# Kernel tuning notes

Hardware: AMD Instinct MI355X
Metric: run time of the kernel (lower is better)

The kernel has to match this reference:

```python
import jax, jax.numpy as jnp
import numpy as np

B, N_FIELDS, D_IN, HID, HEADS = 1024, 32, 64, 128, 4
E_PER_G = 256
N_TOTAL = B * N_FIELDS


def setup_inputs() -> dict:
    key = jax.random.key(0)
    ks = jax.random.split(key, 12)
    # per-graph template edges, replicated with per-graph node offsets
    src_t = jax.random.randint(ks[0], (E_PER_G,), 0, N_FIELDS)
    dst_t = jax.random.randint(ks[1], (E_PER_G,), 0, N_FIELDS)
    offs = (jnp.arange(B) * N_FIELDS)[:, None]
    src = (src_t[None, :] + offs).reshape(-1)
    dst = (dst_t[None, :] + offs).reshape(-1)
    loops = jnp.arange(N_TOTAL)  # PyG GATConv add_self_loops=True
    edge_index = jnp.stack([jnp.concatenate([src, loops]),
                            jnp.concatenate([dst, loops])]).astype(jnp.int32)
    batch_idx = jnp.repeat(jnp.arange(B), N_FIELDS).astype(jnp.int32)

    def glorot(k, shape):
        fan = shape[0]
        return jax.random.normal(k, shape, jnp.float32) / np.float32(np.sqrt(fan))

    return {
        "x_fields": jax.random.normal(ks[2], (B, N_FIELDS, D_IN), jnp.float32),
        "aligner_w": glorot(ks[3], (D_IN, HID)),
        "aligner_b": jnp.zeros((HID,), jnp.float32),
        "ln_gamma": jnp.ones((HID,), jnp.float32),
        "ln_beta": jnp.zeros((HID,), jnp.float32),
        "gate_logits": jnp.full((N_FIELDS,), 2.2, jnp.float32),
        "w1": glorot(ks[4], (HID, HEADS * HID)),
        "att_src1": jax.random.normal(ks[5], (HEADS, HID), jnp.float32) * 0.1,
        "att_dst1": jax.random.normal(ks[6], (HEADS, HID), jnp.float32) * 0.1,
        "bias1": jnp.zeros((HEADS * HID,), jnp.float32),
        "w2": glorot(ks[7], (HEADS * HID, HID)),
        "att_src2": jax.random.normal(ks[8], (1, HID), jnp.float32) * 0.1,
        "att_dst2": jax.random.normal(ks[9], (1, HID), jnp.float32) * 0.1,
        "bias2": jnp.zeros((HID,), jnp.float32),
        "edge_index": edge_index,
        "batch_idx": batch_idx,
    }


def _gat(x, W, a_src, a_dst, bias, src, dst, heads, out_dim, concat):
    n = x.shape[0]
    h = (x @ W).reshape(n, heads, out_dim)          # [N,H,F]
    e_s = jnp.einsum('nhf,hf->nh', h, a_src)         # per-node src logits
    e_d = jnp.einsum('nhf,hf->nh', h, a_dst)
    logits = jax.nn.leaky_relu(e_s[src] + e_d[dst], 0.2)   # [E,H]
    # segment softmax over destination nodes (self-loops -> no empty segs)
    m = jax.ops.segment_max(logits, dst, num_segments=n)
    ex = jnp.exp(logits - m[dst])
    denom = jax.ops.segment_sum(ex, dst, num_segments=n)
    alpha = ex / denom[dst]
    out = jax.ops.segment_sum(h[src] * alpha[..., None], dst, num_segments=n)
    out = out.reshape(n, heads * out_dim) if concat else out.mean(axis=1)
    return out + bias


def reference(x_fields, aligner_w, aligner_b, ln_gamma, ln_beta, gate_logits,
              w1, att_src1, att_dst1, bias1, w2, att_src2, att_dst2, bias2,
              edge_index, batch_idx):
    # fused alignment: one Linear over all fields
    aligned = x_fields @ aligner_w + aligner_b       # [B,N,HID]
    mu = aligned.mean(-1, keepdims=True)
    var = ((aligned - mu) ** 2).mean(-1, keepdims=True)
    normed = (aligned - mu) / jnp.sqrt(var + 1e-5) * ln_gamma + ln_beta
    gate = jax.nn.sigmoid(gate_logits)               # [N]
    x = (normed * gate[None, :, None]).reshape(-1, HID)  # [B*N, HID]
    src, dst = edge_index[0], edge_index[1]
    x = _gat(x, w1, att_src1, att_dst1, bias1, src, dst, HEADS, HID, True)
    x = jax.nn.elu(x)
    x = _gat(x, w2, att_src2, att_dst2, bias2, src, dst, 1, HID, False)
    counts = jax.ops.segment_sum(jnp.ones((x.shape[0],), x.dtype), batch_idx,
                                 num_segments=B)
    graph_embedding = jax.ops.segment_sum(x, batch_idx, num_segments=B) / counts[:, None]
    return graph_embedding, gate
```

## Files before the change

kernel.cpp:

```cpp
#include <hip/hip_runtime.h>
#include <hip/hip_bf16.h>
#include <cstdint>
#include <cstddef>

#define NB    1024
#define NF    32
#define DIN   64
#define HID   128
#define HEADS 4
#define NTOT  (NB*NF)
#define H1DIM (HEADS*HID)

typedef __attribute__((ext_vector_type(8))) short          bf16x8;
typedef __attribute__((ext_vector_type(8))) unsigned short u16x8;
typedef __attribute__((ext_vector_type(4))) float          f32x4;

__device__ __forceinline__ float bf2f(unsigned short u) {
    return __uint_as_float(((unsigned)u) << 16);
}
__device__ __forceinline__ unsigned short f2bf(float f) {
    unsigned u = __float_as_uint(f);
    return (unsigned short)((u + 0x7FFF + ((u >> 16) & 1)) >> 16);
}

__device__ __forceinline__ int x0_at(int r, int c) {
    return r * 128 + ((((c >> 3) ^ (r & 7)) & 15) << 3) + (c & 7);
}
__device__ __forceinline__ int h1_at(int f, int s) {
    return f * 32 + ((((s >> 3) ^ ((f >> 1) & 3)) & 3) << 3) + (s & 7);
}
__device__ __forceinline__ int x1_at(int r, int c) {
    return r * 512 + ((((c >> 3) ^ ((r >> 1) & 7)) & 63) << 3) + (c & 7);
}
__device__ __forceinline__ int al_at(int rr, int s) {
    return rr * 32 + ((((s >> 3) ^ ((rr >> 1) & 3)) & 3) << 3) + (s & 7);
}

__global__ __launch_bounds__(256) void k_prep(
    const float* __restrict__ w1, const float* __restrict__ w2,
    const float* __restrict__ Wa,
    unsigned short* __restrict__ w1T, unsigned short* __restrict__ w2T,
    unsigned short* __restrict__ WaT)
{
    int i = blockIdx.x * 256 + threadIdx.x;
    if (i < HID * H1DIM) {
        int n = i >> 7, k = i & 127;
        w1T[i] = f2bf(w1[k * H1DIM + n]);
    } else if (i < 2 * HID * H1DIM) {
        int j = i - HID * H1DIM;
        int n = j >> 9, k = j & 511;
        w2T[j] = f2bf(w2[k * HID + n]);
    } else {
        int j = i - 2 * HID * H1DIM;
        int c = j >> 6, k = j & 63;
        WaT[j] = f2bf(Wa[k * HID + c]);
    }
}

__global__ __launch_bounds__(256, 3) void k_mega(
    const float* __restrict__ xf, const unsigned short* __restrict__ WaT,
    const float* __restrict__ ba, const float* __restrict__ gamma,
    const float* __restrict__ beta, const float* __restrict__ gl,
    const unsigned short* __restrict__ w1T, const float* __restrict__ as1,
    const float* __restrict__ ad1, const float* __restrict__ b1,
    const unsigned short* __restrict__ w2T, const float* __restrict__ as2,
    const float* __restrict__ ad2, const float* __restrict__ b2,
    const int* __restrict__ src, const int* __restrict__ dst, int epg,
    float* __restrict__ dout)
{
    __shared__ __align__(16) char S[54144];
    int*            cntI   = (int*)S;
    unsigned short* h1T    = (unsigned short*)S;
    unsigned short* x1L    = (unsigned short*)S;
    unsigned short* alphaL = (unsigned short*)(S + 32768);
    unsigned short* x0L    = (unsigned short*)(S + 40960);
    float*          aL2    = (float*)(S + 40960);
    unsigned char*  cntB   = (unsigned char*)(S + 49152);
    float* lnS   = (float*)(S + 50176);
    float* lnS2  = (float*)(S + 50688);
    float* esL   = (float*)(S + 51200);
    float* edL   = (float*)(S + 51712);
    float* rsumL = (float*)(S + 52224);
    float* es2p  = (float*)(S + 52736);
    float* ed2p  = (float*)(S + 53248);
    float* sc2   = (float*)(S + 53760);

    const int b = blockIdx.x, t = threadIdx.x;
    const int l = t & 63, w = t >> 6;
    const int g = l >> 4, i16 = l & 15;
    const int nb = b * NF;
    const f32x4 zf4 = {0.f, 0.f, 0.f, 0.f};

    for (int i = t; i < NF * NF; i += 256) cntI[i] = 0;
    __syncthreads();
    for (int i = t; i < epg; i += 256) {
        int sv = src[b * epg + i] - nb;
        int dv = dst[b * epg + i] - nb;
        atomicAdd(&cntI[dv * NF + sv], 1);
    }
    if (t < NF) atomicAdd(&cntI[t * NF + t], 1);
    __syncthreads();
    for (int i = t; i < NF * NF; i += 256) {
        int c = cntI[i];
        cntB[i] = (unsigned char)(c > 255 ? 255 : c);
    }
    __syncthreads();

    f32x4 accA[2][2];
    #pragma unroll
    for (int m = 0; m < 2; ++m)
        #pragma unroll
        for (int n = 0; n < 2; ++n) accA[m][n] = zf4;

    #pragma unroll
    for (int k = 0; k < 2; ++k) {
        bf16x8 aF[2];
        #pragma unroll
        for (int m = 0; m < 2; ++m) {
            const float* p = &xf[(size_t)(nb + m * 16 + i16) * DIN + k * 32 + g * 8];
            float4 f0 = *(const float4*)p;
            float4 f1 = *(const float4*)(p + 4);
            u16x8 v;
            v[0] = f2bf(f0.x); v[1] = f2bf(f0.y); v[2] = f2bf(f0.z); v[3] = f2bf(f0.w);
            v[4] = f2bf(f1.x); v[5] = f2bf(f1.y); v[6] = f2bf(f1.z); v[7] = f2bf(f1.w);
            aF[m] = (bf16x8)v;
        }
        #pragma unroll
        for (int n = 0; n < 2; ++n) {
            bf16x8 bF = *(const bf16x8*)&WaT[(size_t)(w * 32 + n * 16 + i16) * DIN + k * 32 + g * 8];
            #pragma unroll
            for (int m = 0; m < 2; ++m)
                accA[m][n] = __builtin_amdgcn_mfma_f32_16x16x32_bf16(aF[m], bF, accA[m][n], 0, 0, 0);
        }
    }
    float val[2][2][4];
    float bav[2];
    #pragma unroll
    for (int n = 0; n < 2; ++n) bav[n] = ba[w * 32 + n * 16 + i16];
    float ps[2][4], ps2[2][4];
    #pragma unroll
    for (int m = 0; m < 2; ++m)
        #pragma unroll
        for (int v = 0; v < 4; ++v) {
            float a0 = accA[m][0][v] + bav[0];
            float a1 = accA[m][1][v] + bav[1];
            val[m][0][v] = a0; val[m][1][v] = a1;
            ps[m][v] = a0 + a1;
            ps2[m][v] = a0 * a0 + a1 * a1;
        }
    #pragma unroll
    for (int o = 1; o < 16; o <<= 1) {
        #pragma unroll
        for (int m = 0; m < 2; ++m)
            #pragma unroll
            for (int v = 0; v < 4; ++v) {
                ps[m][v]  += __shfl_xor(ps[m][v], o);
                ps2[m][v] += __shfl_xor(ps2[m][v], o);
            }
    }
    if (i16 == 0) {
        #pragma unroll
        for (int m = 0; m < 2; ++m)
            #pragma unroll
            for (int v = 0; v < 4; ++v) {
                int r = m * 16 + g * 4 + v;
                lnS[w * 32 + r]  = ps[m][v];
                lnS2[w * 32 + r] = ps2[m][v];
            }
    }
    __syncthreads();
    #pragma unroll
    for (int m = 0; m < 2; ++m)
        #pragma unroll
        for (int v = 0; v < 4; ++v) {
            int r = m * 16 + g * 4 + v;
            float S1 = lnS[r] + lnS[32 + r] + lnS[64 + r] + lnS[96 + r];
            float S2 = lnS2[r] + lnS2[32 + r] + lnS2[64 + r] + lnS2[96 + r];
            float mu = S1 * (1.0f / HID);
            float var = S2 * (1.0f / HID) - mu * mu;
            float rs = rsqrtf(var + 1e-5f);
            float gt = 1.0f / (1.0f + __expf(-gl[r]));
            #pragma unroll
            for (int n = 0; n < 2; ++n) {
                int c = w * 32 + n * 16 + i16;
                float xv = ((val[m][n][v] - mu) * rs * gamma[c] + beta[c]) * gt;
                x0L[x0_at(r, c)] = f2bf(xv);
            }
        }
    __syncthreads();

    f32x4 acc1[2][8];
    #pragma unroll
    for (int m = 0; m < 2; ++m)
        #pragma unroll
        for (int n = 0; n < 8; ++n) acc1[m][n] = zf4;

    #pragma unroll 2
    for (int k = 0; k < 4; ++k) {
        bf16x8 aF[2];
        #pragma unroll
        for (int m = 0; m < 2; ++m)
            aF[m] = *(const bf16x8*)&x0L[x0_at(m * 16 + i16, k * 32 + g * 8)];
        #pragma unroll
        for (int n = 0; n < 8; ++n) {
            bf16x8 bF = *(const bf16x8*)&w1T[(size_t)(w * 128 + n * 16 + i16) * 128 + k * 32 + g * 8];
            #pragma unroll
            for (int m = 0; m < 2; ++m)
                acc1[m][n] = __builtin_amdgcn_mfma_f32_16x16x32_bf16(aF[m], bF, acc1[m][n], 0, 0, 0);
        }
    }
    {
        float asv[8], adv[8];
        #pragma unroll
        for (int n = 0; n < 8; ++n) {
            int f = n * 16 + i16;
            asv[n] = as1[w * 128 + f];
            adv[n] = ad1[w * 128 + f];
        }
        float pe[2][4], pd[2][4];
        #pragma unroll
        for (int m = 0; m < 2; ++m)
            #pragma unroll
            for (int v = 0; v < 4; ++v) {
                float e = 0.f, d = 0.f;
                #pragma unroll
                for (int n = 0; n < 8; ++n) {
                    e = fmaf(acc1[m][n][v], asv[n], e);
                    d = fmaf(acc1[m][n][v], adv[n], d);
                }
                pe[m][v] = e; pd[m][v] = d;
            }
        #pragma unroll
        for (int o = 1; o < 16; o <<= 1) {
            #pragma unroll
            for (int m = 0; m < 2; ++m)
                #pragma unroll
                for (int v = 0; v < 4; ++v) {
                    pe[m][v] += __shfl_xor(pe[m][v], o);
                    pd[m][v] += __shfl_xor(pd[m][v], o);
                }
        }
        if (i16 == 0) {
            #pragma unroll
            for (int m = 0; m < 2; ++m)
                #pragma unroll
                for (int v = 0; v < 4; ++v) {
                    int r = m * 16 + g * 4 + v;
                    esL[w * 32 + r] = pe[m][v];
                    edL[w * 32 + r] = pd[m][v];
                }
        }
        #pragma unroll
        for (int m = 0; m < 2; ++m)
            #pragma unroll
            for (int n = 0; n < 8; ++n) {
                int f = w * 128 + n * 16 + i16;
                int s0 = m * 16 + g * 4;
                unsigned d0 = (unsigned)f2bf(acc1[m][n][0]) | ((unsigned)f2bf(acc1[m][n][1]) << 16);
                unsigned d1 = (unsigned)f2bf(acc1[m][n][2]) | ((unsigned)f2bf(acc1[m][n][3]) << 16);
                uint2 pk = {d0, d1};
                *(uint2*)&h1T[h1_at(f, s0)] = pk;
            }
    }
    __syncthreads();

    if (t < 128) {
        int d = t >> 2, h = t & 3;
        float edv = edL[h * 32 + d];
        float mx = -INFINITY;
        #pragma unroll
        for (int s = 0; s < NF; ++s) {
            if (cntB[d * NF + s]) {
                float lg = esL[h * 32 + s] + edv;
                lg = fmaxf(lg, 0.2f * lg);
                mx = fmaxf(mx, lg);
            }
        }
        float sum = 0.f;
        #pragma unroll
        for (int s = 0; s < NF; ++s) {
            int c = cntB[d * NF + s];
            float a = 0.f;
            if (c) {
                float lg = esL[h * 32 + s] + edv;
                lg = fmaxf(lg, 0.2f * lg);
                a = (float)c * __expf(lg - mx);
                sum += a;
            }
            alphaL[al_at(h * 32 + d, s)] = f2bf(a);
        }
        rsumL[h * 32 + d] = 1.0f / sum;
    }
    __syncthreads();

    f32x4 po[2][8];
    {
        bf16x8 aF2[2];
        #pragma unroll
        for (int m = 0; m < 2; ++m)
            aF2[m] = *(const bf16x8*)&alphaL[al_at(w * 32 + m * 16 + i16, g * 8)];
        #pragma unroll
        for (int n = 0; n < 8; ++n) {
            bf16x8 bF = *(const bf16x8*)&h1T[h1_at(w * 128 + n * 16 + i16, g * 8)];
            #pragma unroll
            for (int m = 0; m < 2; ++m)
                po[m][n] = __builtin_amdgcn_mfma_f32_16x16x32_bf16(aF2[m], bF, zf4, 0, 0, 0);
        }
    }
    __syncthreads();
    #pragma unroll
    for (int m = 0; m < 2; ++m)
        #pragma unroll
        for (int n = 0; n < 8; ++n) {
            int c = w * 128 + n * 16 + i16;
            float bias = b1[c];
            #pragma unroll
            for (int v = 0; v < 4; ++v) {
                int r = m * 16 + g * 4 + v;
                float x = po[m][n][v] * rsumL[w * 32 + r] + bias;
                x = (x > 0.f) ? x : (__expf(x) - 1.0f);
                x1L[x1_at(r, c)] = f2bf(x);
            }
        }
    __syncthreads();

    f32x4 acc2[2][2];
    #pragma unroll
    for (int m = 0; m < 2; ++m)
        #pragma unroll
        for (int n = 0; n < 2; ++n) acc2[m][n] = zf4;

    #pragma unroll 4
    for (int k = 0; k < 16; ++k) {
        bf16x8 aF[2];
        #pragma unroll
        for (int m = 0; m < 2; ++m)
            aF[m] = *(const bf16x8*)&x1L[x1_at(m * 16 + i16, k * 32 + g * 8)];
        #pragma unroll
        for (int n = 0; n < 2; ++n) {
            bf16x8 bF = *(const bf16x8*)&w2T[(size_t)(w * 32 + n * 16 + i16) * 512 + k * 32 + g * 8];
            #pragma unroll
            for (int m = 0; m < 2; ++m)
                acc2[m][n] = __builtin_amdgcn_mfma_f32_16x16x32_bf16(aF[m], bF, acc2[m][n], 0, 0, 0);
        }
    }
    {
        float a2v[2], d2v[2];
        #pragma unroll
        for (int n = 0; n < 2; ++n) {
            int c = w * 32 + n * 16 + i16;
            a2v[n] = as2[c]; d2v[n] = ad2[c];
        }
        float pe[2][4], pd[2][4];
        #pragma unroll
        for (int m = 0; m < 2; ++m)
            #pragma unroll
            for (int v = 0; v < 4; ++v) {
                float e = 0.f, d = 0.f;
                #pragma unroll
                for (int n = 0; n < 2; ++n) {
                    e = fmaf(acc2[m][n][v], a2v[n], e);
                    d = fmaf(acc2[m][n][v], d2v[n], d);
                }
                pe[m][v] = e; pd[m][v] = d;
            }
        #pragma unroll
        for (int o = 1; o < 16; o <<= 1) {
            #pragma unroll
            for (int m = 0; m < 2; ++m)
                #pragma unroll
                for (int v = 0; v < 4; ++v) {
                    pe[m][v] += __shfl_xor(pe[m][v], o);
                    pd[m][v] += __shfl_xor(pd[m][v], o);
                }
        }
        if (i16 == 0) {
            #pragma unroll
            for (int m = 0; m < 2; ++m)
                #pragma unroll
                for (int v = 0; v < 4; ++v) {
                    int r = m * 16 + g * 4 + v;
                    es2p[w * 32 + r] = pe[m][v];
                    ed2p[w * 32 + r] = pd[m][v];
                }
        }
    }
    __syncthreads();

    float* es2L = sc2;
    float* ed2L = sc2 + 32;
    float* wn2  = sc2 + 64;
    if (t < NF) {
        es2L[t] = es2p[t] + es2p[32 + t] + es2p[64 + t] + es2p[96 + t];
        ed2L[t] = ed2p[t] + ed2p[32 + t] + ed2p[64 + t] + ed2p[96 + t];
    }
    __syncthreads();
    if (t < NF) {
        int d = t;
        float edv = ed2L[d];
        float mx = -INFINITY;
        #pragma unroll
        for (int s = 0; s < NF; ++s) {
            if (cntB[d * NF + s]) {
                float lg = es2L[s] + edv;
                lg = fmaxf(lg, 0.2f * lg);
                mx = fmaxf(mx, lg);
            }
        }
        float sum = 0.f;
        #pragma unroll
        for (int s = 0; s < NF; ++s) {
            int c = cntB[d * NF + s];
            float a = 0.f;
            if (c) {
                float lg = es2L[s] + edv;
                lg = fmaxf(lg, 0.2f * lg);
                a = (float)c * __expf(lg - mx);
                sum += a;
            }
            aL2[d * 33 + s] = a;
        }
        float rs = 1.0f / sum;
        #pragma unroll
        for (int s = 0; s < NF; ++s) aL2[d * 33 + s] *= rs;
    }
    __syncthreads();
    if (t < NF) {
        float a = 0.f;
        #pragma unroll
        for (int d = 0; d < NF; ++d) a += aL2[d * 33 + t];
        wn2[t] = a;
    }
    __syncthreads();

    {
        float wr_[2][4];
        #pragma unroll
        for (int m = 0; m < 2; ++m)
            #pragma unroll
            for (int v = 0; v < 4; ++v) wr_[m][v] = wn2[m * 16 + g * 4 + v];
        float pl[2];
        #pragma unroll
        for (int n = 0; n < 2; ++n) {
            float a = 0.f;
            #pragma unroll
            for (int m = 0; m < 2; ++m)
                #pragma unroll
                for (int v = 0; v < 4; ++v)
                    a = fmaf(wr_[m][v], acc2[m][n][v], a);
            pl[n] = a;
        }
        #pragma unroll
        for (int n = 0; n < 2; ++n) {
            pl[n] += __shfl_xor(pl[n], 16);
            pl[n] += __shfl_xor(pl[n], 32);
        }
        if (l < 16) {
            #pragma unroll
            for (int n = 0; n < 2; ++n) {
                int c = w * 32 + n * 16 + l;
                dout[(size_t)b * HID + c] = pl[n] * (1.0f / NF) + b2[c];
            }
        }
    }
    if (b == 0 && t < NF)
        dout[(size_t)NB * HID + t] = 1.0f / (1.0f + __expf(-gl[t]));
}

extern "C" void kernel_launch(void* const* d_in, const int* in_sizes, int n_in,
                              void* d_out, int out_size, void* d_ws, size_t ws_size,
                              hipStream_t stream)
{
    const float* xf    = (const float*)d_in[0];
    const float* Wa    = (const float*)d_in[1];
    const float* ba    = (const float*)d_in[2];
    const float* gamma = (const float*)d_in[3];
    const float* beta  = (const float*)d_in[4];
    const float* gl    = (const float*)d_in[5];
    const float* w1    = (const float*)d_in[6];
    const float* as1   = (const float*)d_in[7];
    const float* ad1   = (const float*)d_in[8];
    const float* b1    = (const float*)d_in[9];
    const float* w2    = (const float*)d_in[10];
    const float* as2   = (const float*)d_in[11];
    const float* ad2   = (const float*)d_in[12];
    const float* b2    = (const float*)d_in[13];
    const int*   eidx  = (const int*)d_in[14];
    const int E = in_sizes[14] / 2;
    const int* srcG = eidx;
    const int* dstG = eidx + E;
    const int epg = (E - NTOT) / NB;

    char* w = (char*)d_ws;
    unsigned short* w1T = (unsigned short*)w; w += (size_t)H1DIM * HID * 2;
    unsigned short* w2T = (unsigned short*)w; w += (size_t)HID * H1DIM * 2;
    unsigned short* WaT = (unsigned short*)w; w += (size_t)HID * DIN * 2;

    k_prep<<<(2 * HID * H1DIM + DIN * HID) / 256, 256, 0, stream>>>(
        w1, w2, Wa, w1T, w2T, WaT);

    k_mega<<<NB, 256, 0, stream>>>(
        xf, WaT, ba, gamma, beta, gl, w1T, as1, ad1, b1,
        w2T, as2, ad2, b2, srcG, dstG, epg, (float*)d_out);
}
```

Before: 158.8 us.

## Split fused GAT kernel into per-head layer-1 kernel and separate layer-2 kernel

Replaces the single per-graph mega kernel with two kernels. The first runs one 128-thread block per graph and head, recomputing the aligner and LayerNorm for each head, and writes the ELU output of GAT layer 1 to a global bf16 buffer. The second reads that buffer back for layer 2 and pooling. Both kernels spread the softmax across 128 threads using shuffle reductions, where previously only 32 or 128 threads did the serial loops. The aim is more blocks, smaller LDS use and higher occupancy, at the cost of redundant aligner and edge-count work per head and a global round trip of the 512-wide intermediate.

Result: slower. 164.7 us (+3.7%).

```diff
diff --git a/kernel.cpp b/kernel.cpp
--- a/kernel.cpp
+++ b/kernel.cpp
@@ -26,14 +26,14 @@
 __device__ __forceinline__ int x0_at(int r, int c) {
     return r * 128 + ((((c >> 3) ^ (r & 7)) & 15) << 3) + (c & 7);
 }
-__device__ __forceinline__ int h1_at(int f, int s) {
+__device__ __forceinline__ int hT_at(int f, int s) {
     return f * 32 + ((((s >> 3) ^ ((f >> 1) & 3)) & 3) << 3) + (s & 7);
+}
+__device__ __forceinline__ int al_at(int d, int s) {
+    return d * 32 + ((((s >> 3) ^ ((d >> 1) & 3)) & 3) << 3) + (s & 7);
 }
 __device__ __forceinline__ int x1_at(int r, int c) {
     return r * 512 + ((((c >> 3) ^ ((r >> 1) & 7)) & 63) << 3) + (c & 7);
-}
-__device__ __forceinline__ int al_at(int rr, int s) {
-    return rr * 32 + ((((s >> 3) ^ ((rr >> 1) & 3)) & 3) << 3) + (s & 7);
 }
 
 __global__ __launch_bounds__(256) void k_prep(
@@ -57,60 +57,55 @@
     }
 }
 
-__global__ __launch_bounds__(256, 3) void k_mega(
+__global__ __launch_bounds__(128) void k_gnn1(
     const float* __restrict__ xf, const unsigned short* __restrict__ WaT,
     const float* __restrict__ ba, const float* __restrict__ gamma,
     const float* __restrict__ beta, const float* __restrict__ gl,
     const unsigned short* __restrict__ w1T, const float* __restrict__ as1,
     const float* __restrict__ ad1, const float* __restrict__ b1,
-    const unsigned short* __restrict__ w2T, const float* __restrict__ as2,
-    const float* __restrict__ ad2, const float* __restrict__ b2,
     const int* __restrict__ src, const int* __restrict__ dst, int epg,
-    float* __restrict__ dout)
+    unsigned short* __restrict__ x1g)
 {
-    __shared__ __align__(16) char S[54144];
-    int*            cntI   = (int*)S;
+    __shared__ __align__(16) char S[14592];
+    unsigned short* x0L    = (unsigned short*)S;
     unsigned short* h1T    = (unsigned short*)S;
-    unsigned short* x1L    = (unsigned short*)S;
-    unsigned short* alphaL = (unsigned short*)(S + 32768);
-    unsigned short* x0L    = (unsigned short*)(S + 40960);
-    float*          aL2    = (float*)(S + 40960);
-    unsigned char*  cntB   = (unsigned char*)(S + 49152);
-    float* lnS   = (float*)(S + 50176);
-    float* lnS2  = (float*)(S + 50688);
-    float* esL   = (float*)(S + 51200);
-    float* edL   = (float*)(S + 51712);
-    float* rsumL = (float*)(S + 52224);
-    float* es2p  = (float*)(S + 52736);
-    float* ed2p  = (float*)(S + 53248);
-    float* sc2   = (float*)(S + 53760);
-
-    const int b = blockIdx.x, t = threadIdx.x;
-    const int l = t & 63, w = t >> 6;
+    unsigned short* x1Ls   = (unsigned short*)S;
+    int*            cntI   = (int*)(S + 8192);
+    unsigned short* alphaL = (unsigned short*)(S + 10240);
+    unsigned char*  cntB   = (unsigned char*)(S + 12288);
+    float* lnSp  = (float*)(S + 13312);
+    float* lnS2p = (float*)(S + 13568);
+    float* esP   = (float*)(S + 13824);
+    float* edP   = (float*)(S + 14080);
+    float* rsumL = (float*)(S + 14336);
+
+    const int bid = blockIdx.x;
+    const int b = bid >> 2, h = bid & 3;
+    const int t = threadIdx.x;
+    const int w2 = t >> 6, l = t & 63;
     const int g = l >> 4, i16 = l & 15;
     const int nb = b * NF;
     const f32x4 zf4 = {0.f, 0.f, 0.f, 0.f};
 
-    for (int i = t; i < NF * NF; i += 256) cntI[i] = 0;
-    __syncthreads();
-    for (int i = t; i < epg; i += 256) {
+    for (int i = t; i < NF * NF; i += 128) cntI[i] = 0;
+    __syncthreads();
+    for (int i = t; i < epg; i += 128) {
         int sv = src[b * epg + i] - nb;
         int dv = dst[b * epg + i] - nb;
         atomicAdd(&cntI[dv * NF + sv], 1);
     }
-    if (t < NF) atomicAdd(&cntI[t * NF + t], 1);
-    __syncthreads();
-    for (int i = t; i < NF * NF; i += 256) {
+    if (t < NF) atomicAdd(&cntI[t * 33], 1);
+    __syncthreads();
+    for (int i = t; i < NF * NF; i += 128) {
         int c = cntI[i];
         cntB[i] = (unsigned char)(c > 255 ? 255 : c);
     }
-    __syncthreads();
-
-    f32x4 accA[2][2];
+
+    f32x4 accA[2][4];
     #pragma unroll
     for (int m = 0; m < 2; ++m)
         #pragma unroll
-        for (int n = 0; n < 2; ++n) accA[m][n] = zf4;
+        for (int n = 0; n < 4; ++n) accA[m][n] = zf4;
 
     #pragma unroll
     for (int k = 0; k < 2; ++k) {
@@ -126,28 +121,31 @@
             aF[m] = (bf16x8)v;
         }
         #pragma unroll
-        for (int n = 0; n < 2; ++n) {
-            bf16x8 bF = *(const bf16x8*)&WaT[(size_t)(w * 32 + n * 16 + i16) * DIN + k * 32 + g * 8];
+        for (int n = 0; n < 4; ++n) {
+            bf16x8 bF = *(const bf16x8*)&WaT[(size_t)(w2 * 64 + n * 16 + i16) * DIN + k * 32 + g * 8];
             #pragma unroll
             for (int m = 0; m < 2; ++m)
                 accA[m][n] = __builtin_amdgcn_mfma_f32_16x16x32_bf16(aF[m], bF, accA[m][n], 0, 0, 0);
         }
     }
-    float val[2][2][4];
-    float bav[2];
-    #pragma unroll
-    for (int n = 0; n < 2; ++n) bav[n] = ba[w * 32 + n * 16 + i16];
+    float val[2][4][4];
     float ps[2][4], ps2[2][4];
     #pragma unroll
     for (int m = 0; m < 2; ++m)
         #pragma unroll
-        for (int v = 0; v < 4; ++v) {
-            float a0 = accA[m][0][v] + bav[0];
-            float a1 = accA[m][1][v] + bav[1];
-            val[m][0][v] = a0; val[m][1][v] = a1;
-            ps[m][v] = a0 + a1;
-            ps2[m][v] = a0 * a0 + a1 * a1;
-        }
+        for (int v = 0; v < 4; ++v) { ps[m][v] = 0.f; ps2[m][v] = 0.f; }
+    #pragma unroll
+    for (int n = 0; n < 4; ++n) {
+        float bav = ba[w2 * 64 + n * 16 + i16];
+        #pragma unroll
+        for (int m = 0; m < 2; ++m)
+            #pragma unroll
+            for (int v = 0; v < 4; ++v) {
+                float a = accA[m][n][v] + bav;
+                val[m][n][v] = a;
+                ps[m][v] += a; ps2[m][v] += a * a;
+            }
+    }
     #pragma unroll
     for (int o = 1; o < 16; o <<= 1) {
         #pragma unroll
@@ -164,8 +162,8 @@
             #pragma unroll
             for (int v = 0; v < 4; ++v) {
                 int r = m * 16 + g * 4 + v;
-                lnS[w * 32 + r]  = ps[m][v];
-                lnS2[w * 32 + r] = ps2[m][v];
+                lnSp[w2 * 32 + r]  = ps[m][v];
+                lnS2p[w2 * 32 + r] = ps2[m][v];
             }
     }
     __syncthreads();
@@ -174,48 +172,49 @@
         #pragma unroll
         for (int v = 0; v < 4; ++v) {
             int r = m * 16 + g * 4 + v;
-            float S1 = lnS[r] + lnS[32 + r] + lnS[64 + r] + lnS[96 + r];
-            float S2 = lnS2[r] + lnS2[32 + r] + lnS2[64 + r] + lnS2[96 + r];
+            float S1 = lnSp[r] + lnSp[32 + r];
+            float S2 = lnS2p[r] + lnS2p[32 + r];
             float mu = S1 * (1.0f / HID);
             float var = S2 * (1.0f / HID) - mu * mu;
             float rs = rsqrtf(var + 1e-5f);
             float gt = 1.0f / (1.0f + __expf(-gl[r]));
             #pragma unroll
-            for (int n = 0; n < 2; ++n) {
-                int c = w * 32 + n * 16 + i16;
+            for (int n = 0; n < 4; ++n) {
+                int c = w2 * 64 + n * 16 + i16;
                 float xv = ((val[m][n][v] - mu) * rs * gamma[c] + beta[c]) * gt;
                 x0L[x0_at(r, c)] = f2bf(xv);
             }
         }
     __syncthreads();
 
-    f32x4 acc1[2][8];
+    f32x4 acc1[2][4];
     #pragma unroll
     for (int m = 0; m < 2; ++m)
         #pragma unroll
-        for (int n = 0; n < 8; ++n) acc1[m][n] = zf4;
-
-    #pragma unroll 2
+        for (int n = 0; n < 4; ++n) acc1[m][n] = zf4;
+
+    #pragma unroll
     for (int k = 0; k < 4; ++k) {
         bf16x8 aF[2];
         #pragma unroll
         for (int m = 0; m < 2; ++m)
             aF[m] = *(const bf16x8*)&x0L[x0_at(m * 16 + i16, k * 32 + g * 8)];
         #pragma unroll
-        for (int n = 0; n < 8; ++n) {
-            bf16x8 bF = *(const bf16x8*)&w1T[(size_t)(w * 128 + n * 16 + i16) * 128 + k * 32 + g * 8];
+        for (int n = 0; n < 4; ++n) {
+            bf16x8 bF = *(const bf16x8*)&w1T[(size_t)(h * 128 + w2 * 64 + n * 16 + i16) * 128 + k * 32 + g * 8];
             #pragma unroll
             for (int m = 0; m < 2; ++m)
                 acc1[m][n] = __builtin_amdgcn_mfma_f32_16x16x32_bf16(aF[m], bF, acc1[m][n], 0, 0, 0);
         }
     }
+    __syncthreads();
+
     {
-        float asv[8], adv[8];
-        #pragma unroll
-        for (int n = 0; n < 8; ++n) {
-            int f = n * 16 + i16;
-            asv[n] = as1[w * 128 + f];
-            adv[n] = ad1[w * 128 + f];
+        float asv[4], adv[4];
+        #pragma unroll
+        for (int n = 0; n < 4; ++n) {
+            int f = h * 128 + w2 * 64 + n * 16 + i16;
+            asv[n] = as1[f]; adv[n] = ad1[f];
         }
         float pe[2][4], pd[2][4];
         #pragma unroll
@@ -224,7 +223,7 @@
             for (int v = 0; v < 4; ++v) {
                 float e = 0.f, d = 0.f;
                 #pragma unroll
-                for (int n = 0; n < 8; ++n) {
+                for (int n = 0; n < 4; ++n) {
                     e = fmaf(acc1[m][n][v], asv[n], e);
                     d = fmaf(acc1[m][n][v], adv[n], d);
                 }
@@ -246,82 +245,145 @@
                 #pragma unroll
                 for (int v = 0; v < 4; ++v) {
                     int r = m * 16 + g * 4 + v;
-                    esL[w * 32 + r] = pe[m][v];
-                    edL[w * 32 + r] = pd[m][v];
+                    esP[w2 * 32 + r] = pe[m][v];
+                    edP[w2 * 32 + r] = pd[m][v];
                 }
         }
         #pragma unroll
         for (int m = 0; m < 2; ++m)
             #pragma unroll
-            for (int n = 0; n < 8; ++n) {
-                int f = w * 128 + n * 16 + i16;
+            for (int n = 0; n < 4; ++n) {
+                int f = w2 * 64 + n * 16 + i16;
                 int s0 = m * 16 + g * 4;
                 unsigned d0 = (unsigned)f2bf(acc1[m][n][0]) | ((unsigned)f2bf(acc1[m][n][1]) << 16);
                 unsigned d1 = (unsigned)f2bf(acc1[m][n][2]) | ((unsigned)f2bf(acc1[m][n][3]) << 16);
                 uint2 pk = {d0, d1};
-                *(uint2*)&h1T[h1_at(f, s0)] = pk;
-            }
-    }
-    __syncthreads();
-
-    if (t < 128) {
-        int d = t >> 2, h = t & 3;
-        float edv = edL[h * 32 + d];
+                *(uint2*)&h1T[hT_at(f, s0)] = pk;
+            }
+    }
+    __syncthreads();
+
+    {
+        int d = t >> 2, q = t & 3;
+        float edv = edP[d] + edP[32 + d];
         float mx = -INFINITY;
         #pragma unroll
-        for (int s = 0; s < NF; ++s) {
+        for (int j = 0; j < 8; ++j) {
+            int s = q * 8 + j;
             if (cntB[d * NF + s]) {
-                float lg = esL[h * 32 + s] + edv;
+                float lg = esP[s] + esP[32 + s] + edv;
                 lg = fmaxf(lg, 0.2f * lg);
                 mx = fmaxf(mx, lg);
             }
         }
+        mx = fmaxf(mx, __shfl_xor(mx, 1));
+        mx = fmaxf(mx, __shfl_xor(mx, 2));
         float sum = 0.f;
-        #pragma unroll
-        for (int s = 0; s < NF; ++s) {
+        u16x8 av;
+        #pragma unroll
+        for (int j = 0; j < 8; ++j) {
+            int s = q * 8 + j;
             int c = cntB[d * NF + s];
             float a = 0.f;
             if (c) {
-                float lg = esL[h * 32 + s] + edv;
+                float lg = esP[s] + esP[32 + s] + edv;
                 lg = fmaxf(lg, 0.2f * lg);
                 a = (float)c * __expf(lg - mx);
                 sum += a;
             }
-            alphaL[al_at(h * 32 + d, s)] = f2bf(a);
-        }
-        rsumL[h * 32 + d] = 1.0f / sum;
-    }
-    __syncthreads();
-
-    f32x4 po[2][8];
+            av[j] = f2bf(a);
+        }
+        *(u16x8*)&alphaL[al_at(d, q * 8)] = av;
+        sum += __shfl_xor(sum, 1);
+        sum += __shfl_xor(sum, 2);
+        if (q == 0) rsumL[d] = 1.0f / sum;
+    }
+    __syncthreads();
+
+    f32x4 po[2][4];
     {
         bf16x8 aF2[2];
         #pragma unroll
         for (int m = 0; m < 2; ++m)
-            aF2[m] = *(const bf16x8*)&alphaL[al_at(w * 32 + m * 16 + i16, g * 8)];
-        #pragma unroll
-        for (int n = 0; n < 8; ++n) {
-            bf16x8 bF = *(const bf16x8*)&h1T[h1_at(w * 128 + n * 16 + i16, g * 8)];
+            aF2[m] = *(const bf16x8*)&alphaL[al_at(m * 16 + i16, g * 8)];
+        #pragma unroll
+        for (int n = 0; n < 4; ++n) {
+            bf16x8 bF = *(const bf16x8*)&h1T[hT_at(w2 * 64 + n * 16 + i16, g * 8)];
             #pragma unroll
             for (int m = 0; m < 2; ++m)
                 po[m][n] = __builtin_amdgcn_mfma_f32_16x16x32_bf16(aF2[m], bF, zf4, 0, 0, 0);
         }
     }
     __syncthreads();
+
     #pragma unroll
     for (int m = 0; m < 2; ++m)
         #pragma unroll
-        for (int n = 0; n < 8; ++n) {
-            int c = w * 128 + n * 16 + i16;
-            float bias = b1[c];
+        for (int n = 0; n < 4; ++n) {
+            int c = w2 * 64 + n * 16 + i16;
+            float bias = b1[h * 128 + c];
             #pragma unroll
             for (int v = 0; v < 4; ++v) {
                 int r = m * 16 + g * 4 + v;
-                float x = po[m][n][v] * rsumL[w * 32 + r] + bias;
+                float x = po[m][n][v] * rsumL[r] + bias;
                 x = (x > 0.f) ? x : (__expf(x) - 1.0f);
-                x1L[x1_at(r, c)] = f2bf(x);
-            }
-        }
+                x1Ls[r * 136 + c] = f2bf(x);
+            }
+        }
+    __syncthreads();
+
+    #pragma unroll
+    for (int j = 0; j < 4; ++j) {
+        int cidx = j * 128 + t;
+        int r = cidx >> 4, ch = cidx & 15;
+        u16x8 vv = *(const u16x8*)&x1Ls[r * 136 + ch * 8];
+        *(u16x8*)&x1g[(size_t)(nb + r) * H1DIM + h * 128 + ch * 8] = vv;
+    }
+}
+
+__global__ __launch_bounds__(256) void k_gnn2(
+    const unsigned short* __restrict__ x1g, const unsigned short* __restrict__ w2T,
+    const float* __restrict__ as2, const float* __restrict__ ad2,
+    const float* __restrict__ b2, const float* __restrict__ gl,
+    const int* __restrict__ src, const int* __restrict__ dst, int epg,
+    float* __restrict__ dout)
+{
+    __shared__ __align__(16) char S[39424];
+    unsigned short* x1L  = (unsigned short*)S;
+    int*            cntI = (int*)(S + 32768);
+    float*          aL2  = (float*)(S + 32768);
+    unsigned char*  cntB = (unsigned char*)(S + 37120);
+    float* esP = (float*)(S + 38144);
+    float* edP = (float*)(S + 38656);
+    float* rs2 = (float*)(S + 39168);
+    float* wn2 = (float*)(S + 39296);
+
+    const int b = blockIdx.x, t = threadIdx.x;
+    const int w = t >> 6, l = t & 63;
+    const int g = l >> 4, i16 = l & 15;
+    const int nb = b * NF;
+    const f32x4 zf4 = {0.f, 0.f, 0.f, 0.f};
+
+    for (int i = t; i < NF * NF; i += 256) cntI[i] = 0;
+    __syncthreads();
+    for (int i = t; i < epg; i += 256) {
+        int sv = src[b * epg + i] - nb;
+        int dv = dst[b * epg + i] - nb;
+        atomicAdd(&cntI[dv * NF + sv], 1);
+    }
+    if (t < NF) atomicAdd(&cntI[t * 33], 1);
+    __syncthreads();
+    for (int i = t; i < NF * NF; i += 256) {
+        int c = cntI[i];
+        cntB[i] = (unsigned char)(c > 255 ? 255 : c);
+    }
+    #pragma unroll
+    for (int j = 0; j < 8; ++j) {
+        int idx = j * 256 + t;
+        int r = idx >> 6, ch = idx & 63;
+        u16x8 vv = *(const u16x8*)&x1g[(size_t)(nb + r) * H1DIM + ch * 8];
+        *(u16x8*)&x1L[x1_at(r, ch * 8)] = vv;
+    }
     __syncthreads();
 
     f32x4 acc2[2][2];
@@ -338,7 +400,7 @@
             aF[m] = *(const bf16x8*)&x1L[x1_at(m * 16 + i16, k * 32 + g * 8)];
         #pragma unroll
         for (int n = 0; n < 2; ++n) {
-            bf16x8 bF = *(const bf16x8*)&w2T[(size_t)(w * 32 + n * 16 + i16) * 512 + k * 32 + g * 8];
+            bf16x8 bF = *(const bf16x8*)&w2T[(size_t)(w * 32 + n * 16 + i16) * H1DIM + k * 32 + g * 8];
             #pragma unroll
             for (int m = 0; m < 2; ++m)
                 acc2[m][n] = __builtin_amdgcn_mfma_f32_16x16x32_bf16(aF[m], bF, acc2[m][n], 0, 0, 0);
@@ -380,56 +442,59 @@
                 #pragma unroll
                 for (int v = 0; v < 4; ++v) {
                     int r = m * 16 + g * 4 + v;
-                    es2p[w * 32 + r] = pe[m][v];
-                    ed2p[w * 32 + r] = pd[m][v];
+                    esP[w * 32 + r] = pe[m][v];
+                    edP[w * 32 + r] = pd[m][v];
                 }
         }
     }
     __syncthreads();
 
-    float* es2L = sc2;
-    float* ed2L = sc2 + 32;
-    float* wn2  = sc2 + 64;
-    if (t < NF) {
-        es2L[t] = es2p[t] + es2p[32 + t] + es2p[64 + t] + es2p[96 + t];
-        ed2L[t] = ed2p[t] + ed2p[32 + t] + ed2p[64 + t] + ed2p[96 + t];
-    }
-    __syncthreads();
-    if (t < NF) {
-        int d = t;
-        float edv = ed2L[d];
+    if (t < 128) {
+        int d = t >> 2, q = t & 3;
+        float edv = edP[d] + edP[32 + d] + edP[64 + d] + edP[96 + d];
         float mx = -INFINITY;
         #pragma unroll
-        for (int s = 0; s < NF; ++s) {
+        for (int j = 0; j < 8; ++j) {
+            int s = q * 8 + j;
             if (cntB[d * NF + s]) {
-                float lg = es2L[s] + edv;
+                float lg = esP[s] + esP[32 + s] + esP[64 + s] + esP[96 + s] + edv;
                 lg = fmaxf(lg, 0.2f * lg);
                 mx = fmaxf(mx, lg);
             }
         }
+        mx = fmaxf(mx, __shfl_xor(mx, 1));
+        mx = fmaxf(mx, __shfl_xor(mx, 2));
         float sum = 0.f;
         #pragma unroll
-        for (int s = 0; s < NF; ++s) {
+        for (int j = 0; j < 8; ++j) {
+            int s = q * 8 + j;
             int c = cntB[d * NF + s];
             float a = 0.f;
             if (c) {
-                float lg = es2L[s] + edv;
+                float lg = esP[s] + esP[32 + s] + esP[64 + s] + esP[96 + s] + edv;
                 lg = fmaxf(lg, 0.2f * lg);
                 a = (float)c * __expf(lg - mx);
                 sum += a;
             }
             aL2[d * 33 + s] = a;
         }
-        float rs = 1.0f / sum;
-        #pragma unroll
-        for (int s = 0; s < NF; ++s) aL2[d * 33 + s] *= rs;
-    }
-    __syncthreads();
-    if (t < NF) {
-        float a = 0.f;
-        #pragma unroll
-        for (int d = 0; d < NF; ++d) a += aL2[d * 33 + t];
-        wn2[t] = a;
+        sum += __shfl_xor(sum, 1);
+        sum += __shfl_xor(sum, 2);
+        if (q == 0) rs2[d] = 1.0f / sum;
+    }
+    __syncthreads();
+
+    if (t < 128) {
+        int s = t >> 2, dq = t & 3;
+        float p = 0.f;
+        #pragma unroll
+        for (int j = 0; j < 8; ++j) {
+            int d = dq * 8 + j;
+            p = fmaf(aL2[d * 33 + s], rs2[d], p);
+        }
+        p += __shfl_xor(p, 1);
+        p += __shfl_xor(p, 2);
+        if (dq == 0) wn2[s] = p;
     }
     __syncthreads();
 
@@ -495,11 +560,15 @@
     unsigned short* w1T = (unsigned short*)w; w += (size_t)H1DIM * HID * 2;
     unsigned short* w2T = (unsigned short*)w; w += (size_t)HID * H1DIM * 2;
     unsigned short* WaT = (unsigned short*)w; w += (size_t)HID * DIN * 2;
+    unsigned short* x1g = (unsigned short*)w; w += (size_t)NTOT * H1DIM * 2;
 
     k_prep<<<(2 * HID * H1DIM + DIN * HID) / 256, 256, 0, stream>>>(
         w1, w2, Wa, w1T, w2T, WaT);
 
-    k_mega<<<NB, 256, 0, stream>>>(
+    k_gnn1<<<NB * HEADS, 128, 0, stream>>>(
         xf, WaT, ba, gamma, beta, gl, w1T, as1, ad1, b1,
-        w2T, as2, ad2, b2, srcG, dstG, epg, (float*)d_out);
-}
+        srcG, dstG, epg, x1g);
+
+    k_gnn2<<<NB, 256, 0, stream>>>(
+        x1g, w2T, as2, ad2, b2, gl, srcG, dstG, epg, (float*)d_out);
+}
```
